# Optimization experiments

Measured on AMD Instinct MI355X. Metric: run time of the kernel, lower is better.

## Reference

```python
import jax, jax.numpy as jnp
import numpy as np

LN_EPS = 1e-5
C = 128
N = 512

def _layernorm(x, w, b):
    mu = jnp.mean(x, axis=-1, keepdims=True)
    var = jnp.mean(jnp.square(x - mu), axis=-1, keepdims=True)
    return (x - mu) * jax.lax.rsqrt(var + LN_EPS) * w + b

def setup_inputs() -> dict:
    key = jax.random.key(0)
    ks = jax.random.split(key, 8)
    s_in = 1.0 / np.sqrt(C)
    return {
        "pair": jax.random.normal(ks[0], (N, N, C), dtype=jnp.float32),
        "mask": jnp.ones((N, N), dtype=jnp.float32),
        "ln1_w": jnp.ones((C,), dtype=jnp.float32),
        "ln1_b": jnp.zeros((C,), dtype=jnp.float32),
        "Wp": jax.random.uniform(ks[1], (2 * C, C), jnp.float32, -s_in, s_in),
        "Wg": jax.random.uniform(ks[2], (2 * C, C), jnp.float32, -s_in, s_in),
        "ln2_w": jnp.ones((C,), dtype=jnp.float32),
        "ln2_b": jnp.zeros((C,), dtype=jnp.float32),
        "Wo": jax.random.uniform(ks[3], (C, C), jnp.float32, -s_in, s_in),
        "Wgl": jax.random.uniform(ks[4], (C, C), jnp.float32, -s_in, s_in),
    }

def reference(pair, mask, ln1_w, ln1_b, Wp, Wg, ln2_w, ln2_b, Wo, Wgl):
    # pair: [N, N, C]; mask: [N, N]
    x = _layernorm(pair, ln1_w, ln1_b)                      # left_norm_input
    proj = x @ Wp.T                                          # [N, N, 2C]
    gate = x @ Wg.T                                          # [N, N, 2C]
    proj = proj * mask[:, :, None] * jax.nn.sigmoid(gate)    # masked, gated
    # torch reshape [2C,N,N] -> [C,2,N,N] interleaves channels: a=even, b=odd
    a = proj[..., 0::2]                                      # [N, N, C]
    b = proj[..., 1::2]                                      # [N, N, C]
    # outgoing: 'cik,cjk->cij' with channel-first a,b == 'ikc,jkc->ijc' here
    tri = jnp.einsum('ikc,jkc->ijc', a, b)                   # [N, N, C]
    y = _layernorm(tri, ln2_w, ln2_b)                        # center_norm
    y = y @ Wo.T                                             # output_projection
    y = y * jax.nn.sigmoid(x @ Wgl.T)                        # output gating
    return pair + y
```

## Files before the change

kernel.cpp:

```cpp
#include <hip/hip_runtime.h>
#include <hip/hip_bf16.h>
#include <stdint.h>


#define NN 512
#define CC 128

typedef __attribute__((ext_vector_type(4))) float f32x4;
typedef __attribute__((ext_vector_type(8))) short bf16x8v;

__device__ __forceinline__ uint16_t f2bf(float f) {
  uint32_t u = __builtin_bit_cast(uint32_t, f);
  uint32_t r = u + 0x7fffu + ((u >> 16) & 1u);
  return (uint16_t)(r >> 16);
}
__device__ __forceinline__ float bf2f(uint16_t h) {
  uint32_t u = ((uint32_t)h) << 16;
  return __builtin_bit_cast(float, u);
}
__device__ __forceinline__ float sigmoidf_(float x) {
  return 1.0f / (1.0f + __expf(-x));
}
__device__ __forceinline__ bf16x8v ldbf8(const uint16_t* p) {
  return *reinterpret_cast<const bf16x8v*>(p);
}
#define MFMA16(a, b, c) __builtin_amdgcn_mfma_f32_16x16x32_bf16((a), (b), (c), 0, 0, 0)

__global__ __launch_bounds__(128) void k_pack(const float* __restrict__ Wp,
                                              const float* __restrict__ Wg,
                                              const float* __restrict__ Wgl,
                                              const float* __restrict__ Wo,
                                              uint16_t* __restrict__ Wc) {
  int u = blockIdx.x;
  int k = threadIdx.x;
  const float* src;
  if (u < 512) {
    int q = u >> 2, sel = u & 3;
    int row = 2 * q + ((sel >> 1) & 1);
    src = ((sel & 1) ? Wg : Wp) + row * CC;
  } else if (u < 640) {
    src = Wgl + (u - 512) * CC;
  } else {
    src = Wo + (u - 640) * CC;
  }
  Wc[u * CC + k] = f2bf(src[k]);
}

__global__ __launch_bounds__(256) void k1(
    const float* __restrict__ pair, const float* __restrict__ mask,
    const float* __restrict__ ln1w, const float* __restrict__ ln1b,
    const uint16_t* __restrict__ Wc,
    uint16_t* __restrict__ a_t, uint16_t* __restrict__ b_t,
    uint16_t* __restrict__ gbuf) {
  __shared__ uint16_t x_s[32][136];
  __shared__ float mask_s[32];
  const int t = threadIdx.x;
  const int i = blockIdx.x >> 4;
  const int k0 = (blockIdx.x & 15) << 5;

  {
    const int row = t >> 3, seg = t & 7;
    const float* src = pair + (((i << 9) + k0 + row) << 7) + (seg << 4);
    float v[16];
    float s1 = 0.f, s2 = 0.f;
#pragma unroll
    for (int jq = 0; jq < 4; ++jq) {
      f32x4 q = *reinterpret_cast<const f32x4*>(src + 4 * jq);
#pragma unroll
      for (int e = 0; e < 4; ++e) {
        float x = q[e];
        v[jq * 4 + e] = x;
        s1 += x;
        s2 += x * x;
      }
    }
#pragma unroll
    for (int m = 1; m < 8; m <<= 1) {
      s1 += __shfl_xor(s1, m, 8);
      s2 += __shfl_xor(s2, m, 8);
    }
    const float mu = s1 * (1.f / 128.f);
    const float rs = rsqrtf(s2 * (1.f / 128.f) - mu * mu + 1e-5f);
#pragma unroll
    for (int jq = 0; jq < 4; ++jq) {
      ushort4 pk;
#pragma unroll
      for (int e = 0; e < 4; ++e) {
        int c = (seg << 4) + jq * 4 + e;
        float y = (v[jq * 4 + e] - mu) * rs * ln1w[c] + ln1b[c];
        ((uint16_t*)&pk)[e] = f2bf(y);
      }
      *reinterpret_cast<ushort4*>(&x_s[row][(seg << 4) + jq * 4]) = pk;
    }
    if (t < 32) mask_s[t] = mask[(i << 9) + k0 + t];
  }
  __syncthreads();

  const int w = t >> 6, lane = t & 63;
  const int m16 = lane & 15, kg = lane >> 4;

  bf16x8v af[2][4];
#pragma unroll
  for (int mt = 0; mt < 2; ++mt)
#pragma unroll
    for (int ks = 0; ks < 4; ++ks)
      af[mt][ks] =
          *reinterpret_cast<const bf16x8v*>(&x_s[mt * 16 + m16][ks * 32 + kg * 8]);

#pragma unroll
  for (int idx = 0; idx < 8; ++idx) {
    const int nt = 8 * w + idx;
    const int n0 = nt << 4;
    f32x4 acc0 = {0.f, 0.f, 0.f, 0.f};
    f32x4 acc1 = {0.f, 0.f, 0.f, 0.f};
#pragma unroll
    for (int ks = 0; ks < 4; ++ks) {
      bf16x8v bfr = ldbf8(Wc + ((n0 + m16) << 7) + ks * 32 + kg * 8);
      acc0 = MFMA16(af[0][ks], bfr, acc0);
      acc1 = MFMA16(af[1][ks], bfr, acc1);
    }
    const int sel = m16 & 3;
    const int q = (n0 >> 2) + (m16 >> 2);
#pragma unroll
    for (int mt = 0; mt < 2; ++mt) {
      f32x4 A = mt ? acc1 : acc0;
      ushort4 pk;
#pragma unroll
      for (int r = 0; r < 4; ++r) {
        float gp = __shfl_xor(A[r], 1);
        float val = A[r] * mask_s[mt * 16 + kg * 4 + r] * sigmoidf_(gp);
        ((uint16_t*)&pk)[r] = f2bf(val);
      }
      if ((sel & 1) == 0) {
        uint16_t* dst = (sel == 0) ? a_t : b_t;
        const int kpos = k0 + mt * 16 + kg * 4;
        *reinterpret_cast<ushort4*>(&dst[(((i << 7) + q) << 9) + kpos]) = pk;
      }
    }
  }

#pragma unroll
  for (int idx = 0; idx < 2; ++idx) {
    const int nt = 2 * w + idx;
    const int n0 = 512 + (nt << 4);
    f32x4 acc0 = {0.f, 0.f, 0.f, 0.f};
    f32x4 acc1 = {0.f, 0.f, 0.f, 0.f};
#pragma unroll
    for (int ks = 0; ks < 4; ++ks) {
      bf16x8v bfr = ldbf8(Wc + ((n0 + m16) << 7) + ks * 32 + kg * 8);
      acc0 = MFMA16(af[0][ks], bfr, acc0);
      acc1 = MFMA16(af[1][ks], bfr, acc1);
    }
    const int o = (nt << 4) + m16;
#pragma unroll
    for (int mt = 0; mt < 2; ++mt) {
      f32x4 A = mt ? acc1 : acc0;
#pragma unroll
      for (int r = 0; r < 4; ++r) {
        const int cell2 = k0 + mt * 16 + kg * 4 + r;
        gbuf[(((i << 9) + cell2) << 7) + o] = f2bf(sigmoidf_(A[r]));
      }
    }
  }
}

__global__ __launch_bounds__(256) void k2a(const uint16_t* __restrict__ a_t,
                                           const uint16_t* __restrict__ b_t,
                                           uint16_t* __restrict__ tri) {
  const int swz = ((blockIdx.x & 7) << 8) | (blockIdx.x >> 3);
  const int c = swz >> 4, tl = swz & 15;
  const int i0 = (tl >> 2) << 7, j0 = (tl & 3) << 7;
  const int t = threadIdx.x, w = t >> 6, lane = t & 63;
  const int m16 = lane & 15, kg = lane >> 4;
  const int ib = i0 + ((w >> 1) << 6), jb = j0 + ((w & 1) << 6);
  const uint16_t* ap = a_t + ((size_t)(ib + m16) << 16) + (c << 9) + (kg << 3);
  const uint16_t* bp = b_t + ((size_t)(jb + m16) << 16) + (c << 9) + (kg << 3);

  const f32x4 fz = {0.f, 0.f, 0.f, 0.f};
  f32x4 acc[4][4];
#pragma unroll
  for (int mt = 0; mt < 4; ++mt)
#pragma unroll
    for (int nt = 0; nt < 4; ++nt) acc[mt][nt] = fz;

  for (int k = 0; k < 512; k += 32) {
    bf16x8v af[4], bf[4];
#pragma unroll
    for (int mt = 0; mt < 4; ++mt) af[mt] = ldbf8(ap + (mt << 20) + k);
#pragma unroll
    for (int nt = 0; nt < 4; ++nt) bf[nt] = ldbf8(bp + (nt << 20) + k);
#pragma unroll
    for (int mt = 0; mt < 4; ++mt)
#pragma unroll
      for (int nt = 0; nt < 4; ++nt)
        acc[mt][nt] = MFMA16(af[mt], bf[nt], acc[mt][nt]);
  }

  uint16_t* cp = tri + ((size_t)c << 18);
#pragma unroll
  for (int mt = 0; mt < 4; ++mt)
#pragma unroll
    for (int r = 0; r < 4; ++r) {
      const int irow = ib + (mt << 4) + (kg << 2) + r;
#pragma unroll
      for (int nt = 0; nt < 4; ++nt)
        cp[(irow << 9) + jb + (nt << 4) + m16] = f2bf(acc[mt][nt][r]);
    }
}

__global__ __launch_bounds__(512) void k2b(
    const float* __restrict__ pair,
    const float* __restrict__ ln2w, const float* __restrict__ ln2b,
    const uint16_t* __restrict__ Wc,
    const uint16_t* __restrict__ tri,
    const uint16_t* __restrict__ gbuf, float* __restrict__ out) {
  __shared__ uint16_t y_s[256][136];
  __shared__ float2 red[512];
  __shared__ float2 stat[256];
  __shared__ float wln[128], bln[128];

  const int t = threadIdx.x;
  const int i0 = (blockIdx.x >> 5) << 4;
  const int j0 = (blockIdx.x & 31) << 4;
  const int cell = t & 255, ch = t >> 8;
  const int il = cell >> 4, jl = cell & 15;

  if (t < 128) {
    wln[t] = ln2w[t];
    bln[t] = ln2b[t];
  }

  const uint16_t* tp =
      tri + ((size_t)(ch << 6) << 18) + ((i0 + il) << 9) + j0 + jl;
  unsigned short v[64];
  float s1 = 0.f, s2 = 0.f;
#pragma unroll
  for (int cc = 0; cc < 64; ++cc) {
    unsigned short u = tp[(size_t)cc << 18];
    v[cc] = u;
    float f = bf2f(u);
    s1 += f;
    s2 += f * f;
  }
  red[t] = make_float2(s1, s2);
  __syncthreads();
  if (t < 256) {
    float2 p0 = red[t], p1 = red[t + 256];
    float a1 = p0.x + p1.x, a2 = p0.y + p1.y;
    float mu = a1 * (1.f / 128.f);
    float rs = rsqrtf(a2 * (1.f / 128.f) - mu * mu + 1e-5f);
    stat[t] = make_float2(mu, rs);
  }
  __syncthreads();

  {
    const float2 st = stat[cell];
#pragma unroll
    for (int cq = 0; cq < 16; ++cq) {
      ushort4 pk;
#pragma unroll
      for (int e = 0; e < 4; ++e) {
        const int c = (ch << 6) + (cq << 2) + e;
        float y = (bf2f(v[cq * 4 + e]) - st.x) * st.y * wln[c] + bln[c];
        ((unsigned short*)&pk)[e] = f2bf(y);
      }
      *reinterpret_cast<ushort4*>(&y_s[cell][(ch << 6) + (cq << 2)]) = pk;
    }
  }
  __syncthreads();

  const int w = t >> 6, lane = t & 63, m16 = lane & 15, kg = lane >> 4;
  const uint16_t* WoC = Wc + (640 << 7);

  bf16x8v af[2][4];
#pragma unroll
  for (int h = 0; h < 2; ++h) {
    const int mt = w + (h << 3);
#pragma unroll
    for (int ks = 0; ks < 4; ++ks)
      af[h][ks] = *reinterpret_cast<const bf16x8v*>(
          &y_s[(mt << 4) + m16][(ks << 5) + (kg << 3)]);
  }

  const f32x4 fz = {0.f, 0.f, 0.f, 0.f};
#pragma unroll
  for (int nt = 0; nt < 8; ++nt) {
    bf16x8v bw[4];
#pragma unroll
    for (int ks = 0; ks < 4; ++ks)
      bw[ks] = ldbf8(WoC + (((nt << 4) + m16) << 7) + (ks << 5) + (kg << 3));
    f32x4 acc0 = fz, acc1 = fz;
#pragma unroll
    for (int ks = 0; ks < 4; ++ks) {
      acc0 = MFMA16(af[0][ks], bw[ks], acc0);
      acc1 = MFMA16(af[1][ks], bw[ks], acc1);
    }
    const int o = (nt << 4) + m16;
#pragma unroll
    for (int h = 0; h < 2; ++h) {
      const int mt = w + (h << 3);
      f32x4 A = h ? acc1 : acc0;
#pragma unroll
      for (int r = 0; r < 4; ++r) {
        const int off = ((((i0 + mt) << 9) + j0 + (kg << 2) + r) << 7) + o;
        out[off] = pair[off] + A[r] * bf2f(gbuf[off]);
      }
    }
  }
}

__global__ __launch_bounds__(512) void k2(
    const float* __restrict__ pair,
    const float* __restrict__ ln2w, const float* __restrict__ ln2b,
    const uint16_t* __restrict__ Wc,
    const uint16_t* __restrict__ a_t, const uint16_t* __restrict__ b_t,
    const uint16_t* __restrict__ gbuf, float* __restrict__ out) {
  __shared__ uint16_t y_s[128 * 136];
  __shared__ float2 stat[256];
  float2* red = reinterpret_cast<float2*>(y_s);

  const int bidx = blockIdx.x;
  const int nb = ((bidx & 7) << 7) + (bidx >> 3);
  const int i0 = (nb >> 5) << 4;
  const int j0 = (nb & 31) << 4;
  const int t = threadIdx.x, w = t >> 6, lane = t & 63;
  const int m16 = lane & 15, kg = lane >> 4;
  const int cbase = w << 4;

  const uint16_t* ap = a_t + ((((i0 + m16) << 7) + cbase) << 9) + (kg << 3);
  const uint16_t* bp = b_t + ((((j0 + m16) << 7) + cbase) << 9) + (kg << 3);

  const f32x4 fzero = {0.f, 0.f, 0.f, 0.f};
  f32x4 acc[16];
#pragma unroll
  for (int c = 0; c < 16; ++c) acc[c] = fzero;

  for (int k = 0; k < 512; k += 32) {
#pragma unroll
    for (int c = 0; c < 16; ++c) {
      bf16x8v A = ldbf8(ap + (c << 9) + k);
      bf16x8v B = ldbf8(bp + (c << 9) + k);
      acc[c] = MFMA16(A, B, acc[c]);
    }
  }

  {
    float s1[4] = {0.f, 0.f, 0.f, 0.f};
    float s2[4] = {0.f, 0.f, 0.f, 0.f};
#pragma unroll
    for (int c = 0; c < 16; ++c)
#pragma unroll
      for (int r = 0; r < 4; ++r) {
        float xv = acc[c][r];
        s1[r] += xv;
        s2[r] += xv * xv;
      }
#pragma unroll
    for (int r = 0; r < 4; ++r) {
      int cell = ((kg << 2) + r) * 16 + m16;
      red[(w << 8) + cell] = make_float2(s1[r], s2[r]);
    }
  }
  __syncthreads();
  if (t < 256) {
    float a1 = 0.f, a2 = 0.f;
#pragma unroll
    for (int ww = 0; ww < 8; ++ww) {
      float2 p = red[(ww << 8) + t];
      a1 += p.x;
      a2 += p.y;
    }
    float mu = a1 * (1.f / 128.f);
    float rs = rsqrtf(a2 * (1.f / 128.f) - mu * mu + 1e-5f);
    stat[t] = make_float2(mu, rs);
  }
  __syncthreads();

  const uint16_t* WoC = Wc + (640 << 7);

  for (int half = 0; half < 2; ++half) {
    if ((kg >> 1) == half) {
#pragma unroll
      for (int r = 0; r < 4; ++r) {
        const int iOff = (kg << 2) + r;
        const int cellL = ((iOff - (half << 3)) << 4) + m16;
        const float2 st = stat[(iOff << 4) + m16];
#pragma unroll
        for (int jq = 0; jq < 4; ++jq) {
          ushort4 pk;
#pragma unroll
          for (int e = 0; e < 4; ++e) {
            const int c = (jq << 2) + e;
            float y = (acc[c][r] - st.x) * st.y * ln2w[cbase + c] + ln2b[cbase + c];
            ((uint16_t*)&pk)[e] = f2bf(y);
          }
          *reinterpret_cast<ushort4*>(&y_s[cellL * 136 + cbase + (jq << 2)]) = pk;
        }
      }
    }
    __syncthreads();

    const int mt = (half << 3) + w;
    bf16x8v af2[4];
#pragma unroll
    for (int ks = 0; ks < 4; ++ks)
      af2[ks] = *reinterpret_cast<const bf16x8v*>(
          &y_s[(((mt - (half << 3)) << 4) + m16) * 136 + ks * 32 + (kg << 3)]);
    const int i = i0 + mt;
#pragma unroll
    for (int nt = 0; nt < 8; ++nt) {
      f32x4 a2 = fzero;
#pragma unroll
      for (int ks = 0; ks < 4; ++ks) {
        bf16x8v bw = ldbf8(WoC + (((nt << 4) + m16) << 7) + ks * 32 + (kg << 3));
        a2 = MFMA16(af2[ks], bw, a2);
      }
      const int o = (nt << 4) + m16;
#pragma unroll
      for (int r = 0; r < 4; ++r) {
        const int j = j0 + (kg << 2) + r;
        const int off = (((i << 9) + j) << 7) + o;
        out[off] = pair[off] + a2[r] * bf2f(gbuf[off]);
      }
    }
    __syncthreads();
  }
}

extern "C" void kernel_launch(void* const* d_in, const int* in_sizes, int n_in,
                              void* d_out, int out_size, void* d_ws, size_t ws_size,
                              hipStream_t stream) {
  const float* pair = (const float*)d_in[0];
  const float* mask = (const float*)d_in[1];
  const float* ln1w = (const float*)d_in[2];
  const float* ln1b = (const float*)d_in[3];
  const float* Wp = (const float*)d_in[4];
  const float* Wg = (const float*)d_in[5];
  const float* ln2w = (const float*)d_in[6];
  const float* ln2b = (const float*)d_in[7];
  const float* Wo = (const float*)d_in[8];
  const float* Wgl = (const float*)d_in[9];

  uint8_t* ws = (uint8_t*)d_ws;
  uint16_t* Wc = (uint16_t*)(ws);
  uint16_t* a_t = (uint16_t*)(ws + (1 << 18));
  uint16_t* b_t = (uint16_t*)(ws + (1 << 18) + (1ull << 26));
  uint16_t* gb = (uint16_t*)(ws + (1 << 18) + (2ull << 26));
  uint16_t* tri = (uint16_t*)(ws + (1 << 18) + (3ull << 26));
  const size_t NEED = (1 << 18) + (4ull << 26);

  hipLaunchKernelGGL(k_pack, dim3(768), dim3(128), 0, stream, Wp, Wg, Wgl, Wo, Wc);
  hipLaunchKernelGGL(k1, dim3(8192), dim3(256), 0, stream, pair, mask, ln1w, ln1b,
                     Wc, a_t, b_t, gb);
  if (ws_size >= NEED) {
    hipLaunchKernelGGL(k2a, dim3(2048), dim3(256), 0, stream, a_t, b_t, tri);
    hipLaunchKernelGGL(k2b, dim3(1024), dim3(512), 0, stream, pair, ln2w, ln2b,
                       Wc, tri, gb, (float*)d_out);
  } else {
    hipLaunchKernelGGL(k2, dim3(1024), dim3(512), 0, stream, pair, ln2w, ln2b, Wc,
                       a_t, b_t, gb, (float*)d_out);
  }
}
```

Before: 652.3 us.

## Stage triangle GEMM through LDS, repack projection weights, transpose gate buffer

The triangle-multiply kernel now loads A/B tiles into LDS with global_load_lds, double-buffers them across k-steps and uses an XOR swizzle, instead of having each wave issue direct global loads. Projection weights are repacked so each wave computes matching proj and gate tiles together, which removes the cross-lane shuffle and the wasted half of the output stores. The output gate buffer is stored channel-major so both writes and reads become vectorized ushort4 accesses. The layernorm-2 kernel is retiled to do vector reads of tri, and both kernels gain occupancy hints. This adds more LDS use and synchronization.

```diff
diff --git a/kernel.cpp b/kernel.cpp
--- a/kernel.cpp
+++ b/kernel.cpp
@@ -35,9 +35,8 @@
   int k = threadIdx.x;
   const float* src;
   if (u < 512) {
-    int q = u >> 2, sel = u & 3;
-    int row = 2 * q + ((sel >> 1) & 1);
-    src = ((sel & 1) ? Wg : Wp) + row * CC;
+    int tau = u >> 4, r = u & 15, m = tau >> 1;
+    src = ((tau & 1) ? Wg : Wp) + (16 * m + r) * CC;
   } else if (u < 640) {
     src = Wgl + (u - 512) * CC;
   } else {
@@ -51,7 +50,7 @@
     const float* __restrict__ ln1w, const float* __restrict__ ln1b,
     const uint16_t* __restrict__ Wc,
     uint16_t* __restrict__ a_t, uint16_t* __restrict__ b_t,
-    uint16_t* __restrict__ gbuf) {
+    uint16_t* __restrict__ gbuf2) {
   __shared__ uint16_t x_s[32][136];
   __shared__ float mask_s[32];
   const int t = threadIdx.x;
@@ -98,6 +97,7 @@
 
   const int w = t >> 6, lane = t & 63;
   const int m16 = lane & 15, kg = lane >> 4;
+  const f32x4 fz = {0.f, 0.f, 0.f, 0.f};
 
   bf16x8v af[2][4];
 #pragma unroll
@@ -108,34 +108,34 @@
           *reinterpret_cast<const bf16x8v*>(&x_s[mt * 16 + m16][ks * 32 + kg * 8]);
 
 #pragma unroll
-  for (int idx = 0; idx < 8; ++idx) {
-    const int nt = 8 * w + idx;
-    const int n0 = nt << 4;
-    f32x4 acc0 = {0.f, 0.f, 0.f, 0.f};
-    f32x4 acc1 = {0.f, 0.f, 0.f, 0.f};
+  for (int idx = 0; idx < 4; ++idx) {
+    const int m = 4 * w + idx;
+    const uint16_t* wp = Wc + (((2 * m) * 16 + m16) << 7) + kg * 8;
+    const uint16_t* wg = Wc + (((2 * m + 1) * 16 + m16) << 7) + kg * 8;
+    f32x4 ap0 = fz, ap1 = fz, ag0 = fz, ag1 = fz;
 #pragma unroll
     for (int ks = 0; ks < 4; ++ks) {
-      bf16x8v bfr = ldbf8(Wc + ((n0 + m16) << 7) + ks * 32 + kg * 8);
-      acc0 = MFMA16(af[0][ks], bfr, acc0);
-      acc1 = MFMA16(af[1][ks], bfr, acc1);
-    }
-    const int sel = m16 & 3;
-    const int q = (n0 >> 2) + (m16 >> 2);
+      bf16x8v bp = ldbf8(wp + ks * 32);
+      bf16x8v bg = ldbf8(wg + ks * 32);
+      ap0 = MFMA16(af[0][ks], bp, ap0);
+      ap1 = MFMA16(af[1][ks], bp, ap1);
+      ag0 = MFMA16(af[0][ks], bg, ag0);
+      ag1 = MFMA16(af[1][ks], bg, ag1);
+    }
+    const int q = 8 * m + (m16 >> 1);
+    uint16_t* dst = (m16 & 1) ? b_t : a_t;
+    uint16_t* base = dst + (((i << 7) + q) << 9) + k0;
 #pragma unroll
     for (int mt = 0; mt < 2; ++mt) {
-      f32x4 A = mt ? acc1 : acc0;
+      f32x4 P = mt ? ap1 : ap0;
+      f32x4 G = mt ? ag1 : ag0;
       ushort4 pk;
 #pragma unroll
       for (int r = 0; r < 4; ++r) {
-        float gp = __shfl_xor(A[r], 1);
-        float val = A[r] * mask_s[mt * 16 + kg * 4 + r] * sigmoidf_(gp);
+        float val = P[r] * mask_s[mt * 16 + kg * 4 + r] * sigmoidf_(G[r]);
         ((uint16_t*)&pk)[r] = f2bf(val);
       }
-      if ((sel & 1) == 0) {
-        uint16_t* dst = (sel == 0) ? a_t : b_t;
-        const int kpos = k0 + mt * 16 + kg * 4;
-        *reinterpret_cast<ushort4*>(&dst[(((i << 7) + q) << 9) + kpos]) = pk;
-      }
+      *reinterpret_cast<ushort4*>(base + mt * 16 + kg * 4) = pk;
     }
   }
 
@@ -143,39 +143,64 @@
   for (int idx = 0; idx < 2; ++idx) {
     const int nt = 2 * w + idx;
     const int n0 = 512 + (nt << 4);
-    f32x4 acc0 = {0.f, 0.f, 0.f, 0.f};
-    f32x4 acc1 = {0.f, 0.f, 0.f, 0.f};
+    f32x4 a0 = fz, a1 = fz;
 #pragma unroll
     for (int ks = 0; ks < 4; ++ks) {
       bf16x8v bfr = ldbf8(Wc + ((n0 + m16) << 7) + ks * 32 + kg * 8);
-      acc0 = MFMA16(af[0][ks], bfr, acc0);
-      acc1 = MFMA16(af[1][ks], bfr, acc1);
+      a0 = MFMA16(af[0][ks], bfr, a0);
+      a1 = MFMA16(af[1][ks], bfr, a1);
     }
     const int o = (nt << 4) + m16;
+    uint16_t* gb = gbuf2 + (((i << 7) + o) << 9) + k0;
 #pragma unroll
     for (int mt = 0; mt < 2; ++mt) {
-      f32x4 A = mt ? acc1 : acc0;
-#pragma unroll
-      for (int r = 0; r < 4; ++r) {
-        const int cell2 = k0 + mt * 16 + kg * 4 + r;
-        gbuf[(((i << 9) + cell2) << 7) + o] = f2bf(sigmoidf_(A[r]));
-      }
-    }
-  }
-}
-
-__global__ __launch_bounds__(256) void k2a(const uint16_t* __restrict__ a_t,
-                                           const uint16_t* __restrict__ b_t,
-                                           uint16_t* __restrict__ tri) {
+      f32x4 A = mt ? a1 : a0;
+      ushort4 pk;
+#pragma unroll
+      for (int r = 0; r < 4; ++r) ((uint16_t*)&pk)[r] = f2bf(sigmoidf_(A[r]));
+      *reinterpret_cast<ushort4*>(gb + mt * 16 + kg * 4) = pk;
+    }
+  }
+}
+
+__global__ __launch_bounds__(256, 2) void k2a(const uint16_t* __restrict__ a_t,
+                                              const uint16_t* __restrict__ b_t,
+                                              uint16_t* __restrict__ tri) {
+  __shared__ uint16_t ldsAB[32768];
   const int swz = ((blockIdx.x & 7) << 8) | (blockIdx.x >> 3);
   const int c = swz >> 4, tl = swz & 15;
   const int i0 = (tl >> 2) << 7, j0 = (tl & 3) << 7;
   const int t = threadIdx.x, w = t >> 6, lane = t & 63;
   const int m16 = lane & 15, kg = lane >> 4;
-  const int ib = i0 + ((w >> 1) << 6), jb = j0 + ((w & 1) << 6);
-  const uint16_t* ap = a_t + ((size_t)(ib + m16) << 16) + (c << 9) + (kg << 3);
-  const uint16_t* bp = b_t + ((size_t)(jb + m16) << 16) + (c << 9) + (kg << 3);
-
+  const int g = (lane & 7) ^ (lane >> 3);
+
+  const uint16_t* aSrc =
+      a_t + ((size_t)((i0 + (w << 5) + (lane >> 3)) << 7) + c) * 512 + (g << 3);
+  const uint16_t* bSrc =
+      b_t + ((size_t)((j0 + (w << 5) + (lane >> 3)) << 7) + c) * 512 + (g << 3);
+
+#define STAGE(dstbuf, kt)                                                        \
+  {                                                                              \
+    _Pragma("unroll") for (int q = 0; q < 4; ++q) {                              \
+      __builtin_amdgcn_global_load_lds(                                          \
+          (const __attribute__((address_space(1))) void*)(aSrc +                 \
+                                                          ((size_t)q << 19) +    \
+                                                          ((kt) << 6)),          \
+          (__attribute__((address_space(3))) void*)(ldsAB + (dstbuf)*8192 +      \
+                                                    (w << 11) + (q << 9)),       \
+          16, 0, 0);                                                             \
+      __builtin_amdgcn_global_load_lds(                                          \
+          (const __attribute__((address_space(1))) void*)(bSrc +                 \
+                                                          ((size_t)q << 19) +    \
+                                                          ((kt) << 6)),          \
+          (__attribute__((address_space(3))) void*)(ldsAB + 16384 +              \
+                                                    (dstbuf)*8192 + (w << 11) +  \
+                                                    (q << 9)),                   \
+          16, 0, 0);                                                             \
+    }                                                                            \
+  }
+
+  const int wi = (w >> 1) << 6, wj = (w & 1) << 6;
   const f32x4 fz = {0.f, 0.f, 0.f, 0.f};
   f32x4 acc[4][4];
 #pragma unroll
@@ -183,95 +208,135 @@
 #pragma unroll
     for (int nt = 0; nt < 4; ++nt) acc[mt][nt] = fz;
 
-  for (int k = 0; k < 512; k += 32) {
-    bf16x8v af[4], bf[4];
-#pragma unroll
-    for (int mt = 0; mt < 4; ++mt) af[mt] = ldbf8(ap + (mt << 20) + k);
-#pragma unroll
-    for (int nt = 0; nt < 4; ++nt) bf[nt] = ldbf8(bp + (nt << 20) + k);
+  STAGE(0, 0);
+  __syncthreads();
+
+  for (int kt = 0; kt < 8; ++kt) {
+    const int cur = kt & 1;
+    if (kt < 7) STAGE(cur ^ 1, kt + 1);
+    const uint16_t* lA = ldsAB + cur * 8192;
+    const uint16_t* lB = ldsAB + 16384 + cur * 8192;
+    bf16x8v afr[4][2], bfr[4][2];
+#pragma unroll
+    for (int mt = 0; mt < 4; ++mt) {
+      const int R = wi + (mt << 4) + m16;
+      const int rb = R << 6, rx = R & 7;
+#pragma unroll
+      for (int ks = 0; ks < 2; ++ks)
+        afr[mt][ks] = *reinterpret_cast<const bf16x8v*>(
+            &lA[rb + ((((ks << 2) + kg) ^ rx) << 3)]);
+    }
+#pragma unroll
+    for (int nt = 0; nt < 4; ++nt) {
+      const int R = wj + (nt << 4) + m16;
+      const int rb = R << 6, rx = R & 7;
+#pragma unroll
+      for (int ks = 0; ks < 2; ++ks)
+        bfr[nt][ks] = *reinterpret_cast<const bf16x8v*>(
+            &lB[rb + ((((ks << 2) + kg) ^ rx) << 3)]);
+    }
 #pragma unroll
     for (int mt = 0; mt < 4; ++mt)
 #pragma unroll
+      for (int nt = 0; nt < 4; ++nt) {
+        acc[mt][nt] = MFMA16(afr[mt][0], bfr[nt][0], acc[mt][nt]);
+        acc[mt][nt] = MFMA16(afr[mt][1], bfr[nt][1], acc[mt][nt]);
+      }
+    __syncthreads();
+  }
+#undef STAGE
+
+  uint16_t* cp = tri + ((size_t)c << 18);
+#pragma unroll
+  for (int mt = 0; mt < 4; ++mt)
+#pragma unroll
+    for (int r = 0; r < 4; ++r) {
+      const int irow = i0 + wi + (mt << 4) + (kg << 2) + r;
+#pragma unroll
       for (int nt = 0; nt < 4; ++nt)
-        acc[mt][nt] = MFMA16(af[mt], bf[nt], acc[mt][nt]);
-  }
-
-  uint16_t* cp = tri + ((size_t)c << 18);
-#pragma unroll
-  for (int mt = 0; mt < 4; ++mt)
-#pragma unroll
-    for (int r = 0; r < 4; ++r) {
-      const int irow = ib + (mt << 4) + (kg << 2) + r;
-#pragma unroll
-      for (int nt = 0; nt < 4; ++nt)
-        cp[(irow << 9) + jb + (nt << 4) + m16] = f2bf(acc[mt][nt][r]);
-    }
-}
-
-__global__ __launch_bounds__(512) void k2b(
+        cp[(irow << 9) + j0 + wj + (nt << 4) + m16] = f2bf(acc[mt][nt][r]);
+    }
+}
+
+__global__ __launch_bounds__(512, 4) void k2b(
     const float* __restrict__ pair,
     const float* __restrict__ ln2w, const float* __restrict__ ln2b,
     const uint16_t* __restrict__ Wc,
     const uint16_t* __restrict__ tri,
-    const uint16_t* __restrict__ gbuf, float* __restrict__ out) {
-  __shared__ uint16_t y_s[256][136];
-  __shared__ float2 red[512];
+    const uint16_t* __restrict__ gbuf2, float* __restrict__ out) {
+  __shared__ __align__(16) char smem_[256 * 136 * 2];
+  uint16_t(*y_s)[136] = (uint16_t(*)[136])smem_;
+  float2* red = (float2*)smem_;
   __shared__ float2 stat[256];
   __shared__ float wln[128], bln[128];
 
-  const int t = threadIdx.x;
-  const int i0 = (blockIdx.x >> 5) << 4;
-  const int j0 = (blockIdx.x & 31) << 4;
-  const int cell = t & 255, ch = t >> 8;
-  const int il = cell >> 4, jl = cell & 15;
+  const int t = threadIdx.x, bid = blockIdx.x;
+  const int i0 = (bid >> 4) << 3;
+  const int j0 = (bid & 15) << 5;
+  const int w = t >> 6, lane = t & 63;
 
   if (t < 128) {
     wln[t] = ln2w[t];
     bln[t] = ln2b[t];
   }
 
+  const int il = lane >> 3;
+  const int jq4 = (lane & 7) << 2;
   const uint16_t* tp =
-      tri + ((size_t)(ch << 6) << 18) + ((i0 + il) << 9) + j0 + jl;
-  unsigned short v[64];
-  float s1 = 0.f, s2 = 0.f;
-#pragma unroll
-  for (int cc = 0; cc < 64; ++cc) {
-    unsigned short u = tp[(size_t)cc << 18];
-    v[cc] = u;
-    float f = bf2f(u);
-    s1 += f;
-    s2 += f * f;
-  }
-  red[t] = make_float2(s1, s2);
+      tri + ((size_t)(w << 4) << 18) + ((i0 + il) << 9) + j0 + jq4;
+  ushort4 v4[16];
+  float s1[4] = {0.f, 0.f, 0.f, 0.f}, s2[4] = {0.f, 0.f, 0.f, 0.f};
+#pragma unroll
+  for (int cc = 0; cc < 16; ++cc) {
+    ushort4 u = *reinterpret_cast<const ushort4*>(tp + ((size_t)cc << 18));
+    v4[cc] = u;
+#pragma unroll
+    for (int e = 0; e < 4; ++e) {
+      float f = bf2f(((const uint16_t*)&u)[e]);
+      s1[e] += f;
+      s2[e] += f * f;
+    }
+  }
+#pragma unroll
+  for (int e = 0; e < 4; ++e)
+    red[(w << 8) + (il << 5) + jq4 + e] = make_float2(s1[e], s2[e]);
   __syncthreads();
   if (t < 256) {
-    float2 p0 = red[t], p1 = red[t + 256];
-    float a1 = p0.x + p1.x, a2 = p0.y + p1.y;
+    float a1 = 0.f, a2 = 0.f;
+#pragma unroll
+    for (int ww = 0; ww < 8; ++ww) {
+      float2 p = red[(ww << 8) + t];
+      a1 += p.x;
+      a2 += p.y;
+    }
     float mu = a1 * (1.f / 128.f);
     float rs = rsqrtf(a2 * (1.f / 128.f) - mu * mu + 1e-5f);
     stat[t] = make_float2(mu, rs);
   }
   __syncthreads();
 
-  {
+#pragma unroll
+  for (int e = 0; e < 4; ++e) {
+    const int cell = (il << 5) + jq4 + e;
     const float2 st = stat[cell];
 #pragma unroll
-    for (int cq = 0; cq < 16; ++cq) {
+    for (int c4 = 0; c4 < 4; ++c4) {
       ushort4 pk;
 #pragma unroll
-      for (int e = 0; e < 4; ++e) {
-        const int c = (ch << 6) + (cq << 2) + e;
-        float y = (bf2f(v[cq * 4 + e]) - st.x) * st.y * wln[c] + bln[c];
-        ((unsigned short*)&pk)[e] = f2bf(y);
-      }
-      *reinterpret_cast<ushort4*>(&y_s[cell][(ch << 6) + (cq << 2)]) = pk;
-    }
-  }
-  __syncthreads();
-
-  const int w = t >> 6, lane = t & 63, m16 = lane & 15, kg = lane >> 4;
+      for (int d = 0; d < 4; ++d) {
+        const int c = (w << 4) + (c4 << 2) + d;
+        float y =
+            (bf2f(((const uint16_t*)&v4[(c4 << 2) + d])[e]) - st.x) * st.y * wln[c] +
+            bln[c];
+        ((uint16_t*)&pk)[d] = f2bf(y);
+      }
+      *reinterpret_cast<ushort4*>(&y_s[cell][(w << 4) + (c4 << 2)]) = pk;
+    }
+  }
+  __syncthreads();
+
+  const int m16 = lane & 15, kg = lane >> 4;
   const uint16_t* WoC = Wc + (640 << 7);
-
   bf16x8v af[2][4];
 #pragma unroll
   for (int h = 0; h < 2; ++h) {
@@ -300,10 +365,15 @@
     for (int h = 0; h < 2; ++h) {
       const int mt = w + (h << 3);
       f32x4 A = h ? acc1 : acc0;
+      const int cellb = (mt << 4) + (kg << 2);
+      const int i = i0 + (cellb >> 5);
+      const int jb = j0 + (cellb & 31);
+      ushort4 g4 = *reinterpret_cast<const ushort4*>(
+          &gbuf2[(((i << 7) + o) << 9) + jb]);
 #pragma unroll
       for (int r = 0; r < 4; ++r) {
-        const int off = ((((i0 + mt) << 9) + j0 + (kg << 2) + r) << 7) + o;
-        out[off] = pair[off] + A[r] * bf2f(gbuf[off]);
+        const int off = (((i << 9) + jb + r) << 7) + o;
+        out[off] = pair[off] + A[r] * bf2f(((const uint16_t*)&g4)[r]);
       }
     }
   }
@@ -314,7 +384,7 @@
     const float* __restrict__ ln2w, const float* __restrict__ ln2b,
     const uint16_t* __restrict__ Wc,
     const uint16_t* __restrict__ a_t, const uint16_t* __restrict__ b_t,
-    const uint16_t* __restrict__ gbuf, float* __restrict__ out) {
+    const uint16_t* __restrict__ gbuf2, float* __restrict__ out) {
   __shared__ uint16_t y_s[128 * 136];
   __shared__ float2 stat[256];
   float2* red = reinterpret_cast<float2*>(y_s);
@@ -420,7 +490,7 @@
       for (int r = 0; r < 4; ++r) {
         const int j = j0 + (kg << 2) + r;
         const int off = (((i << 9) + j) << 7) + o;
-        out[off] = pair[off] + a2[r] * bf2f(gbuf[off]);
+        out[off] = pair[off] + a2[r] * bf2f(gbuf2[(((i << 7) + o) << 9) + j]);
       }
     }
     __syncthreads();
```

Measured after the change: 608.1 us. -6.8%, faster.
